# Kernel tuning notes

Hardware: AMD Instinct MI355X
Metric: run time of the kernel (lower is better)

The kernel has to match this reference:

```python
import jax, jax.numpy as jnp
import numpy as np

DIM = 256
HEADS = 8
DIM_HEAD = 32
INNER = HEADS * DIM_HEAD
K_NEIGHBORS = 16
TEMPERATURE = 1.0
SCALE = DIM_HEAD ** (-0.5)
BATCH = 512
N_FEATURES = 32


def setup_inputs() -> dict:
    key = jax.random.key(0)
    ks = jax.random.split(key, 6)
    s = 0.02
    return {
        "x": jax.random.normal(ks[0], (BATCH, N_FEATURES, DIM), dtype=jnp.float32),
        "W_qkv": jax.random.normal(ks[1], (DIM, 3 * INNER), dtype=jnp.float32) * s,
        "W_out": jax.random.normal(ks[2], (INNER, DIM), dtype=jnp.float32) * s,
        "b_out": jnp.zeros((DIM,), dtype=jnp.float32),
        "W_repr": jax.random.normal(ks[3], (DIM, DIM), dtype=jnp.float32) * s,
        "b_repr": jnp.zeros((DIM,), dtype=jnp.float32),
    }


def reference(x, W_qkv, W_out, b_out, W_repr, b_repr):
    B, n, d = x.shape
    # A. sample representations: mean over features + linear proj
    reprs = jnp.mean(x, axis=1) @ W_repr + b_repr  # [B, dim]
    # B. kNN graph via cosine similarity
    normed = reprs / jnp.linalg.norm(reprs, axis=-1, keepdims=True)
    sim_mat = (normed @ normed.T) / TEMPERATURE  # [B, B]
    k_actual = min(K_NEIGHBORS + 1, B)
    _, knn_idx = jax.lax.top_k(sim_mat, k_actual)  # [B, k+1]
    # C. attention mask: 0 for self+neighbors, -inf elsewhere
    neg_inf = jnp.float32(-jnp.inf)
    mask = jnp.full((B, B), neg_inf, dtype=jnp.float32)
    mask = mask.at[jnp.arange(B)[:, None], knn_idx].set(0.0)  # [B, B]
    # D. masked cross-sample attention (vectorized over all features/heads)
    qkv = x @ W_qkv  # [B, n, 3*inner]
    q, k, v = jnp.split(qkv, 3, axis=-1)
    def to_bhnd(t):
        return t.reshape(B, n, HEADS, DIM_HEAD).transpose(0, 2, 1, 3)  # b h n d
    q, k, v = to_bhnd(q), to_bhnd(k), to_bhnd(v)
    # per-feature cross-sample scores: [n, b, h, B]
    sim = jnp.einsum('bhnd,Bhnd->nbhB', q, k) * SCALE
    sim = sim + mask[None, :, None, :]
    attn = jax.nn.softmax(sim, axis=-1)
    out = jnp.einsum('nbhB,Bhnd->bnhd', attn, v)  # [b, n, h, d]
    out = out.reshape(B, n, INNER)
    return out @ W_out + b_out
```

## Files before the change

### kernel.cpp

```cpp
#include <hip/hip_runtime.h>
#include <math.h>

#define DIMX 256
#define NFEAT 32
#define BATCH 512
#define HEADS 8
#define DHEAD 32
#define KNN 17
#define QKV_W 768
#define SCALE_L2 0.25503486f

typedef unsigned int uint;
typedef unsigned short ushort_t;
typedef __attribute__((ext_vector_type(8))) short short8_t;
typedef __attribute__((ext_vector_type(4))) float float4_t;

__device__ inline float bf_lo(uint u) { return __uint_as_float(u << 16); }
__device__ inline float bf_hi(uint u) { return __uint_as_float(u & 0xffff0000u); }
__device__ inline ushort_t f2bf(float f) {
  uint u = __float_as_uint(f);
  return (ushort_t)((u + 0x7fffu + ((u >> 16) & 1u)) >> 16);
}

#if defined(__has_builtin)
#if __has_builtin(__builtin_amdgcn_fdot2_f32_bf16)
#define HAVE_DOT2 1
#endif
#if __has_builtin(__builtin_amdgcn_exp2f)
#define EXP2(x) __builtin_amdgcn_exp2f(x)
#endif
#endif
#ifndef EXP2
#define EXP2(x) exp2f(x)
#endif

#ifdef HAVE_DOT2
typedef __attribute__((ext_vector_type(2))) __bf16 bf16x2_t;
__device__ inline float dot2bf(uint a, uint b, float c) {
  return __builtin_amdgcn_fdot2_f32_bf16(
      __builtin_bit_cast(bf16x2_t, a), __builtin_bit_cast(bf16x2_t, b), c, false);
}
#else
__device__ inline float dot2bf(uint a, uint b, float c) {
  return c + bf_lo(a)*bf_lo(b) + bf_hi(a)*bf_hi(b);
}
#endif

__device__ inline void gload16(const ushort_t* g, ushort_t* l) {
  __builtin_amdgcn_global_load_lds(
      (const __attribute__((address_space(1))) void*)g,
      (__attribute__((address_space(3))) void*)l, 16, 0, 0);
}

__global__ __launch_bounds__(256, 2) void repr_prep_kernel(
    const float* __restrict__ x, const float* __restrict__ W_repr,
    const float* __restrict__ b_repr, const float* __restrict__ Wq,
    const float* __restrict__ Wo, float* __restrict__ normed,
    ushort_t* __restrict__ xbf, ushort_t* __restrict__ wqT, ushort_t* __restrict__ woT) {
  __shared__ float smem[64*65];
  int bid = blockIdx.x, t = threadIdx.x;
  if (bid < BATCH) {
    float* mean_s = smem;
    float* red = smem + 256;
    int b = bid;
    float s = 0.f;
#pragma unroll
    for (int n = 0; n < NFEAT; ++n) {
      float v = x[(size_t)(b*NFEAT+n)*DIMX + t];
      s += v;
      xbf[(size_t)(b*NFEAT+n)*DIMX + t] = f2bf(v);
    }
    mean_s[t] = s * (1.0f/NFEAT);
    __syncthreads();
    float a0 = b_repr[t], a1 = 0.f, a2 = 0.f, a3 = 0.f;
#pragma unroll 8
    for (int d = 0; d < 64; ++d) {
      a0 += mean_s[d      ] * W_repr[(d      )*DIMX + t];
      a1 += mean_s[d +  64] * W_repr[(d +  64)*DIMX + t];
      a2 += mean_s[d + 128] * W_repr[(d + 128)*DIMX + t];
      a3 += mean_s[d + 192] * W_repr[(d + 192)*DIMX + t];
    }
    float acc = (a0 + a1) + (a2 + a3);
    red[t] = acc*acc;
    __syncthreads();
    for (int off = 128; off > 0; off >>= 1) {
      if (t < off) red[t] += red[t+off];
      __syncthreads();
    }
    normed[b*DIMX + t] = acc / sqrtf(red[0]);
  } else {
    int pb = bid - BATCH;
    const float* W; ushort_t* WT; int NN, tx, ty;
    if (pb < 48) { W = Wq; WT = wqT; NN = QKV_W; tx = pb % 12; ty = pb / 12; }
    else { int b2 = pb - 48; W = Wo; WT = woT; NN = DIMX; tx = b2 % 4; ty = b2 / 4; }
    float (*tile)[65] = (float(*)[65])smem;
#pragma unroll
    for (int i = 0; i < 4; ++i) {
      int c = t + 256*i;
      int r = c >> 4, c4 = (c & 15) * 4;
      *(float4*)&tile[r][c4] = *(const float4*)&W[(size_t)(ty*64 + r)*NN + tx*64 + c4];
    }
    __syncthreads();
    int rr = t >> 2, cc0 = (t & 3) * 16;
    uint ow[8];
#pragma unroll
    for (int k = 0; k < 8; ++k)
      ow[k] = (uint)f2bf(tile[cc0 + 2*k][rr]) | ((uint)f2bf(tile[cc0 + 2*k + 1][rr]) << 16);
    uint4 o0 = {ow[0], ow[1], ow[2], ow[3]};
    uint4 o1 = {ow[4], ow[5], ow[6], ow[7]};
    size_t obase = (size_t)(tx*64 + rr)*DIMX + ty*64 + cc0;
    *(uint4*)&WT[obase]     = o0;
    *(uint4*)&WT[obase + 8] = o1;
  }
}

template<bool OUTF32>
__device__ __forceinline__ void gemm_body(
    ushort_t (&As)[2][128][64], ushort_t (&Bs)[2][128][64],
    const ushort_t* __restrict__ A, const ushort_t* __restrict__ Bt,
    void* __restrict__ Cout, const float* __restrict__ bias,
    int M, int N, int K, int row0, int col0) {
  int t = threadIdx.x, l = t & 63, w = t >> 6;
  int wr = w >> 1, wc = w & 1;
  int srcRow = l >> 3, srcCol = (l & 7) * 8;
  float4_t acc[4][4] = {};
  int nkt = K >> 6;
#pragma unroll
  for (int i = 0; i < 4; ++i) {
    int ar = w*32 + i*8;
    gload16(&A [(size_t)(row0+ar+srcRow)*K + srcCol], &As[0][ar][0]);
    gload16(&Bt[(size_t)(col0+ar+srcRow)*K + srcCol], &Bs[0][ar][0]);
  }
  __syncthreads();
  int cur = 0;
  for (int kt = 0; kt < nkt; ++kt) {
    if (kt + 1 < nkt) {
      int k1 = (kt + 1) << 6;
#pragma unroll
      for (int i = 0; i < 4; ++i) {
        int ar = w*32 + i*8;
        gload16(&A [(size_t)(row0+ar+srcRow)*K + k1 + srcCol], &As[cur^1][ar][0]);
        gload16(&Bt[(size_t)(col0+ar+srcRow)*K + k1 + srcCol], &Bs[cur^1][ar][0]);
      }
    }
#pragma unroll
    for (int ks = 0; ks < 2; ++ks) {
      int kk = ks*32 + (l >> 4)*8;
      short8_t a[4], b[4];
#pragma unroll
      for (int m = 0; m < 4; ++m) a[m] = *(short8_t*)&As[cur][wr*64 + m*16 + (l & 15)][kk];
#pragma unroll
      for (int n = 0; n < 4; ++n) b[n] = *(short8_t*)&Bs[cur][wc*64 + n*16 + (l & 15)][kk];
#pragma unroll
      for (int m = 0; m < 4; ++m)
#pragma unroll
        for (int n = 0; n < 4; ++n)
          acc[m][n] = __builtin_amdgcn_mfma_f32_16x16x32_bf16(a[m], b[n], acc[m][n], 0, 0, 0);
    }
    __syncthreads();
    cur ^= 1;
  }
  int crow = (l >> 4) * 4, ccol = l & 15;
#pragma unroll
  for (int m = 0; m < 4; ++m)
#pragma unroll
    for (int n = 0; n < 4; ++n) {
      int col = col0 + wc*64 + n*16 + ccol;
#pragma unroll
      for (int r = 0; r < 4; ++r) {
        int row = row0 + wr*64 + m*16 + crow + r;
        if (OUTF32) ((float*)Cout)[(size_t)row*N + col] = acc[m][n][r] + bias[col];
        else        ((ushort_t*)Cout)[(size_t)row*N + col] = f2bf(acc[m][n][r]);
      }
    }
}

template<bool OUTF32>
__global__ __launch_bounds__(256, 2) void mfma_gemm(
    const ushort_t* __restrict__ A, const ushort_t* __restrict__ Bt,
    void* __restrict__ Cout, const float* __restrict__ bias, int M, int N, int K) {
  __shared__ ushort_t As[2][128][64];
  __shared__ ushort_t Bs[2][128][64];
  gemm_body<OUTF32>(As, Bs, A, Bt, Cout, bias, M, N, K, blockIdx.x*128, blockIdx.y*128);
}

__global__ __launch_bounds__(256, 2) void simqkv_kernel(
    const ushort_t* __restrict__ xbf, const ushort_t* __restrict__ wqT,
    ushort_t* __restrict__ qkv, const float* __restrict__ normed,
    float* __restrict__ sims) {
  __shared__ ushort_t As[2][128][64];
  __shared__ ushort_t Bs[2][128][64];
  int bid = blockIdx.x, t = threadIdx.x;
  if (bid < 768) {
    gemm_body<false>(As, Bs, xbf, wqT, qkv, nullptr, 16384, QKV_W, DIMX,
                     (bid & 127) * 128, (bid >> 7) * 128);
  } else {
    int sid = bid - 768;
    int i0 = (sid & 15) * 32, j0 = (sid >> 4) * 32;
    float (*sA)[68] = (float(*)[68])(&As[0][0][0]);
    float (*sB)[68] = (float(*)[68])(&Bs[0][0][0]);
    int tx = t & 15, ty = t >> 4;
    float acc00 = 0.f, acc01 = 0.f, acc10 = 0.f, acc11 = 0.f;
    for (int k0 = 0; k0 < DIMX; k0 += 64) {
#pragma unroll
      for (int c = t; c < 512; c += 256) {
        int r = c >> 4, cc = (c & 15) * 4;
        *(float4*)&sA[r][cc] = *(const float4*)&normed[(size_t)(i0 + r)*DIMX + k0 + cc];
        *(float4*)&sB[r][cc] = *(const float4*)&normed[(size_t)(j0 + r)*DIMX + k0 + cc];
      }
      __syncthreads();
#pragma unroll 16
      for (int kk = 0; kk < 64; ++kk) {
        float a0 = sA[ty*2][kk],   a1 = sA[ty*2+1][kk];
        float b0 = sB[tx*2][kk],   b1 = sB[tx*2+1][kk];
        acc00 += a0*b0; acc01 += a0*b1; acc10 += a1*b0; acc11 += a1*b1;
      }
      __syncthreads();
    }
    sims[(size_t)(i0+ty*2  )*BATCH + j0+tx*2  ] = acc00;
    sims[(size_t)(i0+ty*2  )*BATCH + j0+tx*2+1] = acc01;
    sims[(size_t)(i0+ty*2+1)*BATCH + j0+tx*2  ] = acc10;
    sims[(size_t)(i0+ty*2+1)*BATCH + j0+tx*2+1] = acc11;
  }
}

__global__ __launch_bounds__(256, 8) void topk_rank(const float* __restrict__ sims,
                                                    int* __restrict__ knn) {
  int i = blockIdx.x, t = threadIdx.x;
  __shared__ float row[BATCH];
  row[t]       = sims[(size_t)i*BATCH + t];
  row[t + 256] = sims[(size_t)i*BATCH + t + 256];
  __syncthreads();
  float v1 = row[t], v2 = row[t + 256];
  int i1 = t, i2 = t + 256;
  int r1 = 0, r2 = 0;
  const float4* r4 = (const float4*)row;
#pragma unroll 8
  for (int c = 0; c < BATCH/4; ++c) {
    float4 q = r4[c];
    int base = c * 4;
    r1 += (q.x > v1 || (q.x == v1 && base+0 < i1));
    r1 += (q.y > v1 || (q.y == v1 && base+1 < i1));
    r1 += (q.z > v1 || (q.z == v1 && base+2 < i1));
    r1 += (q.w > v1 || (q.w == v1 && base+3 < i1));
    r2 += (q.x > v2 || (q.x == v2 && base+0 < i2));
    r2 += (q.y > v2 || (q.y == v2 && base+1 < i2));
    r2 += (q.z > v2 || (q.z == v2 && base+2 < i2));
    r2 += (q.w > v2 || (q.w == v2 && base+3 < i2));
  }
  if (r1 < KNN) knn[i*32 + r1] = i1;
  if (r2 < KNN) knn[i*32 + r2] = i2;
}

#define NF_BLK 8
__global__ __launch_bounds__(256, 8) void attn_kernel(
    const ushort_t* __restrict__ qkv, const int* __restrict__ knn,
    ushort_t* __restrict__ attn_out) {
  int b = blockIdx.x, g = blockIdx.y, t = threadIdx.x;
  int n0 = g * NF_BLK;
  __shared__ float sc_s[2][KNN][HEADS];
  __shared__ int idxp[KNN];
  if (t < KNN) idxp[t] = knn[b*32 + t] * (NFEAT*QKV_W);
  __syncthreads();

  for (int np = 0; np < NF_BLK; np += 2) {
    int n = n0 + np;
    for (int job = t; job < 2*KNN*HEADS; job += 256) {
      int f = (job >= KNN*HEADS) ? 1 : 0;
      int r = job - f*KNN*HEADS;
      int j = r >> 3, h = r & 7;
      const uint4* qp = (const uint4*)&qkv[(size_t)(b*NFEAT + n + f)*QKV_W + h*DHEAD];
      const uint4* kp = (const uint4*)&qkv[(size_t)(idxp[j] + (n + f)*QKV_W + 256 + h*DHEAD)];
      float s0 = 0.f, s1 = 0.f;
#pragma unroll
      for (int i = 0; i < 4; ++i) {
        uint4 qv = qp[i], kv = kp[i];
        s0 = dot2bf(kv.x, qv.x, s0); s1 = dot2bf(kv.y, qv.y, s1);
        s0 = dot2bf(kv.z, qv.z, s0); s1 = dot2bf(kv.w, qv.w, s1);
      }
      sc_s[f][j][h] = (s0 + s1) * SCALE_L2;
    }
    __syncthreads();
    {
      int f = t >> 7, p = t & 127, h = p >> 4;
      float sv[KNN];
#pragma unroll
      for (int j = 0; j < KNN; ++j) sv[j] = sc_s[f][j][h];
      float m = sv[0];
#pragma unroll
      for (int j = 1; j < KNN; ++j) m = fmaxf(m, sv[j]);
      float sum = 0.f;
#pragma unroll
      for (int j = 0; j < KNN; ++j) { sv[j] = EXP2(sv[j] - m); sum += sv[j]; }
      float inv = 1.0f / sum;
      int voff = (n + f)*QKV_W + 512 + p*2;
      float alo = 0.f, ahi = 0.f;
#pragma unroll
      for (int j = 0; j < KNN; ++j) {
        uint wv = *(const uint*)&qkv[(size_t)(idxp[j] + voff)];
        alo += sv[j] * bf_lo(wv);
        ahi += sv[j] * bf_hi(wv);
      }
      *(uint*)&attn_out[(size_t)(b*NFEAT + n + f)*DIMX + p*2] =
          (uint)f2bf(alo * inv) | ((uint)f2bf(ahi * inv) << 16);
    }
    __syncthreads();
  }
}

extern "C" void kernel_launch(void* const* d_in, const int* in_sizes, int n_in,
                              void* d_out, int out_size, void* d_ws, size_t ws_size,
                              hipStream_t stream) {
  const float* x      = (const float*)d_in[0];
  const float* W_qkv  = (const float*)d_in[1];
  const float* W_out  = (const float*)d_in[2];
  const float* b_out  = (const float*)d_in[3];
  const float* W_repr = (const float*)d_in[4];
  const float* b_repr = (const float*)d_in[5];
  float* out = (float*)d_out;

  ushort_t* qkv      = (ushort_t*)d_ws;
  ushort_t* xbf      = qkv + (size_t)16384*QKV_W;
  ushort_t* wqT      = xbf + (size_t)16384*DIMX;
  ushort_t* woT      = wqT + (size_t)QKV_W*DIMX;
  ushort_t* attn_out = woT + (size_t)DIMX*DIMX;
  float*    normed   = (float*)(attn_out + (size_t)16384*DIMX);
  float*    sims     = normed + (size_t)BATCH*DIMX;
  int*      knn      = (int*)(sims + (size_t)BATCH*BATCH);

  repr_prep_kernel<<<BATCH + 64, 256, 0, stream>>>(
      x, W_repr, b_repr, W_qkv, W_out, normed, xbf, wqT, woT);
  simqkv_kernel<<<768 + 256, 256, 0, stream>>>(xbf, wqT, qkv, normed, sims);
  topk_rank<<<BATCH, 256, 0, stream>>>(sims, knn);
  attn_kernel<<<dim3(BATCH, NFEAT/NF_BLK), 256, 0, stream>>>(qkv, knn, attn_out);
  mfma_gemm<true><<<dim3(128, 2), 256, 0, stream>>>(
      attn_out, woT, out, b_out, 16384, DIMX, DIMX);
}
```

Measured before the change: 94.31 us.

## Fuse output projection GEMM into attention kernel via LDS tile and MFMA

The attention kernel now keeps its 8-row bf16 output tile in shared memory (padded to 16 rows with zeros) and multiplies it by the transposed W_out directly with MFMA, adding the bias and writing fp32 output. This removes the attn_out round trip through global memory and the separate GEMM launch. In exchange, each block reads all of W_out from global or L2, half the MFMA rows are wasted on padding, and the extra shared memory may reduce occupancy.

Result: slower. 111.0 us (+17.7%).

```diff
diff --git a/kernel.cpp b/kernel.cpp
--- a/kernel.cpp
+++ b/kernel.cpp
@@ -114,12 +114,10 @@
   }
 }
 
-template<bool OUTF32>
 __device__ __forceinline__ void gemm_body(
     ushort_t (&As)[2][128][64], ushort_t (&Bs)[2][128][64],
     const ushort_t* __restrict__ A, const ushort_t* __restrict__ Bt,
-    void* __restrict__ Cout, const float* __restrict__ bias,
-    int M, int N, int K, int row0, int col0) {
+    ushort_t* __restrict__ Cout, int N, int K, int row0, int col0) {
   int t = threadIdx.x, l = t & 63, w = t >> 6;
   int wr = w >> 1, wc = w & 1;
   int srcRow = l >> 3, srcCol = (l & 7) * 8;
@@ -169,19 +167,9 @@
 #pragma unroll
       for (int r = 0; r < 4; ++r) {
         int row = row0 + wr*64 + m*16 + crow + r;
-        if (OUTF32) ((float*)Cout)[(size_t)row*N + col] = acc[m][n][r] + bias[col];
-        else        ((ushort_t*)Cout)[(size_t)row*N + col] = f2bf(acc[m][n][r]);
-      }
-    }
-}
-
-template<bool OUTF32>
-__global__ __launch_bounds__(256, 2) void mfma_gemm(
-    const ushort_t* __restrict__ A, const ushort_t* __restrict__ Bt,
-    void* __restrict__ Cout, const float* __restrict__ bias, int M, int N, int K) {
-  __shared__ ushort_t As[2][128][64];
-  __shared__ ushort_t Bs[2][128][64];
-  gemm_body<OUTF32>(As, Bs, A, Bt, Cout, bias, M, N, K, blockIdx.x*128, blockIdx.y*128);
+        Cout[(size_t)row*N + col] = f2bf(acc[m][n][r]);
+      }
+    }
 }
 
 __global__ __launch_bounds__(256, 2) void simqkv_kernel(
@@ -192,8 +180,7 @@
   __shared__ ushort_t Bs[2][128][64];
   int bid = blockIdx.x, t = threadIdx.x;
   if (bid < 768) {
-    gemm_body<false>(As, Bs, xbf, wqT, qkv, nullptr, 16384, QKV_W, DIMX,
-                     (bid & 127) * 128, (bid >> 7) * 128);
+    gemm_body(As, Bs, xbf, wqT, qkv, QKV_W, DIMX, (bid & 127) * 128, (bid >> 7) * 128);
   } else {
     int sid = bid - 768;
     int i0 = (sid & 15) * 32, j0 = (sid >> 4) * 32;
@@ -253,14 +240,19 @@
 }
 
 #define NF_BLK 8
+#define OLD_STRIDE 264
 __global__ __launch_bounds__(256, 8) void attn_kernel(
     const ushort_t* __restrict__ qkv, const int* __restrict__ knn,
-    ushort_t* __restrict__ attn_out) {
+    const ushort_t* __restrict__ woT, const float* __restrict__ b_out,
+    float* __restrict__ out) {
   int b = blockIdx.x, g = blockIdx.y, t = threadIdx.x;
   int n0 = g * NF_BLK;
   __shared__ float sc_s[2][KNN][HEADS];
   __shared__ int idxp[KNN];
+  __shared__ ushort_t o_lds[16][OLD_STRIDE];
   if (t < KNN) idxp[t] = knn[b*32 + t] * (NFEAT*QKV_W);
+  for (int i = t; i < 8*OLD_STRIDE; i += 256)
+    o_lds[8 + i/OLD_STRIDE][i % OLD_STRIDE] = 0;
   __syncthreads();
 
   for (int np = 0; np < NF_BLK; np += 2) {
@@ -301,10 +293,36 @@
         alo += sv[j] * bf_lo(wv);
         ahi += sv[j] * bf_hi(wv);
       }
-      *(uint*)&attn_out[(size_t)(b*NFEAT + n + f)*DIMX + p*2] =
+      *(uint*)&o_lds[np + f][p*2] =
           (uint)f2bf(alo * inv) | ((uint)f2bf(ahi * inv) << 16);
     }
     __syncthreads();
+  }
+
+  int l = t & 63, w = t >> 6;
+  int arow = l & 15, koff = (l >> 4) * 8;
+  float4_t acc[4] = {};
+#pragma unroll
+  for (int ks = 0; ks < 8; ++ks) {
+    short8_t a = *(short8_t*)&o_lds[arow][ks*32 + koff];
+#pragma unroll
+    for (int nf = 0; nf < 4; ++nf) {
+      short8_t bf = *(const short8_t*)&woT[(size_t)(w*64 + nf*16 + arow)*DIMX + ks*32 + koff];
+      acc[nf] = __builtin_amdgcn_mfma_f32_16x16x32_bf16(a, bf, acc[nf], 0, 0, 0);
+    }
+  }
+  int crow4 = (l >> 4) * 4, ccol = l & 15;
+  if (crow4 < 8) {
+#pragma unroll
+    for (int nf = 0; nf < 4; ++nf) {
+      int col = w*64 + nf*16 + ccol;
+      float bias = b_out[col];
+#pragma unroll
+      for (int r = 0; r < 4; ++r) {
+        int row = crow4 + r;
+        out[(size_t)(b*NFEAT + n0 + row)*DIMX + col] = acc[nf][r] + bias;
+      }
+    }
   }
 }
 
@@ -323,8 +341,7 @@
   ushort_t* xbf      = qkv + (size_t)16384*QKV_W;
   ushort_t* wqT      = xbf + (size_t)16384*DIMX;
   ushort_t* woT      = wqT + (size_t)QKV_W*DIMX;
-  ushort_t* attn_out = woT + (size_t)DIMX*DIMX;
-  float*    normed   = (float*)(attn_out + (size_t)16384*DIMX);
+  float*    normed   = (float*)(woT + (size_t)DIMX*DIMX);
   float*    sims     = normed + (size_t)BATCH*DIMX;
   int*      knn      = (int*)(sims + (size_t)BATCH*BATCH);
 
@@ -332,7 +349,5 @@
       x, W_repr, b_repr, W_qkv, W_out, normed, xbf, wqT, woT);
   simqkv_kernel<<<768 + 256, 256, 0, stream>>>(xbf, wqT, qkv, normed, sims);
   topk_rank<<<BATCH, 256, 0, stream>>>(sims, knn);
-  attn_kernel<<<dim3(BATCH, NFEAT/NF_BLK), 256, 0, stream>>>(qkv, knn, attn_out);
-  mfma_gemm<true><<<dim3(128, 2), 256, 0, stream>>>(
-      attn_out, woT, out, b_out, 16384, DIMX, DIMX);
-}
+  attn_kernel<<<dim3(BATCH, NFEAT/NF_BLK), 256, 0, stream>>>(qkv, knn, woT, b_out, out);
+}
```
